# Optimization experiments

Hardware: AMD Instinct MI355X
Metric: run time of the kernel (lower is better)

The kernel has to match this reference:

```python
import jax, jax.numpy as jnp
import numpy as np

B, L, D = 2, 2048, 1024
H = 16          # num_heads == num_key_value_heads
FD = 16         # feature_dim (q/k head dim)
HD = D // H     # head_dim = 64 (v head dim)
EPS = 1e-5


def setup_inputs() -> dict:
    key = jax.random.key(0)
    k0, k1, k2, k3, k4 = jax.random.split(key, 5)
    scale = 0.02
    return {
        "hidden_states": jax.random.normal(k0, (B, L, D), jnp.float32),
        "Wq": jax.random.normal(k1, (D, H * FD), jnp.float32) * scale,
        "Wk": jax.random.normal(k2, (D, H * FD), jnp.float32) * scale,
        "Wv": jax.random.normal(k3, (D, H * HD), jnp.float32) * scale,
        "Wo": jax.random.normal(k4, (H * HD, D), jnp.float32) * scale,
    }


def reference(hidden_states, Wq, Wk, Wv, Wo):
    # projections (bias-free), split heads: b l (h d) -> b h l d
    q = (hidden_states @ Wq).reshape(B, L, H, FD).transpose(0, 2, 1, 3)
    k = (hidden_states @ Wk).reshape(B, L, H, FD).transpose(0, 2, 1, 3)
    v = (hidden_states @ Wv).reshape(B, L, H, HD).transpose(0, 2, 1, 3)

    # parallel_rebased: squared-dot-product kernel attention, causal,
    # row-normalized by the kernel sum (use_scale=True, use_normalize=True)
    qk_scale = FD ** -0.5
    s = jnp.einsum('bhqd,bhkd->bhqk', q * qk_scale, k)
    s = s * s  # quadratic feature map: (q.k)^2
    causal = jnp.tril(jnp.ones((L, L), dtype=bool))
    s = jnp.where(causal, s, 0.0)
    z = jnp.sum(s, axis=-1)  # [B,H,L]
    o = jnp.einsum('bhqk,bhkd->bhqd', s, v) / (z[..., None] + EPS)

    # merge heads: b h l d -> b l (h d), output projection
    o = o.transpose(0, 2, 1, 3).reshape(B, L, H * HD)
    return o @ Wo
```

## Files before the change

kernel.cpp:

```cpp
#include <hip/hip_runtime.h>
#include <hip/hip_bf16.h>

#define BB 2
#define LL 2048
#define DD 1024
#define HH 16
#define FD 16
#define HD 64
#define EPS 1e-5f
#define RQKV 1536
#define NFIX 4

typedef __attribute__((ext_vector_type(4))) float f32x4;
typedef __attribute__((ext_vector_type(8))) _Float16 f16x8;
typedef __attribute__((ext_vector_type(4))) _Float16 f16x4;

__global__ __launch_bounds__(256) void cast_hs(
    const float* __restrict__ src, _Float16* __restrict__ dst, int n) {
  int idx = (blockIdx.x * 256 + threadIdx.x) * 16;
  if (idx >= n) return;
#pragma unroll
  for (int half = 0; half < 2; half++) {
    float4 a = *(const float4*)(src + idx + half * 8);
    float4 b = *(const float4*)(src + idx + half * 8 + 4);
    f16x8 p = {(_Float16)a.x, (_Float16)a.y, (_Float16)a.z, (_Float16)a.w,
               (_Float16)b.x, (_Float16)b.y, (_Float16)b.z, (_Float16)b.w};
    *(f16x8*)(dst + idx + half * 8) = p;
  }
}

__global__ __launch_bounds__(256) void transpose_qkv(
    const float* __restrict__ Wq, const float* __restrict__ Wk,
    const float* __restrict__ Wv, _Float16* __restrict__ dst) {
  __shared__ _Float16 s[32][40];
  const int ct = blockIdx.x % 48, kt = blockIdx.x / 48;
  const float* src;
  int n0, ncol, drow;
  if (ct < 8) { src = Wq; n0 = ct * 32; ncol = 256; drow = n0; }
  else if (ct < 16) { src = Wk; n0 = (ct - 8) * 32; ncol = 256; drow = 256 + n0; }
  else { src = Wv; n0 = (ct - 16) * 32; ncol = 1024; drow = 512 + n0; }
  const int k0 = kt * 32;
  const int tid = threadIdx.x;
  {
    int r = tid >> 3, c = (tid & 7) * 4;
    float4 v = *(const float4*)(src + (size_t)(k0 + r) * ncol + n0 + c);
    f16x4 p = {(_Float16)v.x, (_Float16)v.y, (_Float16)v.z, (_Float16)v.w};
    *(f16x4*)&s[r][c] = p;
  }
  __syncthreads();
  {
    int n = tid >> 3, kk = (tid & 7) * 4;
    f16x4 o = {s[kk + 0][n], s[kk + 1][n], s[kk + 2][n], s[kk + 3][n]};
    *(f16x4*)(dst + (size_t)(drow + n) * DD + k0 + kk) = o;
  }
}

__global__ __launch_bounds__(256) void transpose_cast(
    const float* __restrict__ src, _Float16* __restrict__ dst, int K, int N) {
  __shared__ _Float16 s[32][40];
  const int n0 = blockIdx.x * 32, k0 = blockIdx.y * 32;
  const int tid = threadIdx.x;
  {
    int r = tid >> 3, c = (tid & 7) * 4;
    float4 v = *(const float4*)(src + (size_t)(k0 + r) * N + n0 + c);
    f16x4 p = {(_Float16)v.x, (_Float16)v.y, (_Float16)v.z, (_Float16)v.w};
    *(f16x4*)&s[r][c] = p;
  }
  __syncthreads();
  {
    int n = tid >> 3, kk = (tid & 7) * 4;
    f16x4 o = {s[kk + 0][n], s[kk + 1][n], s[kk + 2][n], s[kk + 3][n]};
    *(f16x4*)(dst + (size_t)(n0 + n) * K + k0 + kk) = o;
  }
}

template <typename OutT>
__global__ __launch_bounds__(256) void gemm_f16(
    const _Float16* __restrict__ A, const _Float16* __restrict__ Bt,
    OutT* __restrict__ C, int M, int N, int K) {
  constexpr int LDT = 72;
  __shared__ __attribute__((aligned(16))) _Float16 sA[128 * LDT];
  __shared__ __attribute__((aligned(16))) _Float16 sB[128 * LDT];
  const int tid = threadIdx.x;
  const int m0 = blockIdx.y * 128, n0 = blockIdx.x * 128;
  const int w = tid >> 6, lane = tid & 63, quad = lane >> 4, l16 = lane & 15;
  const int wm = (w >> 1) * 64, wn = (w & 1) * 64;

  const int sr = tid >> 1, sh = (tid & 1) * 32;
  const _Float16* Ag = A + (size_t)(m0 + sr) * K + sh;
  const _Float16* Bg = Bt + (size_t)(n0 + sr) * K + sh;
  _Float16* sAw = &sA[sr * LDT + sh];
  _Float16* sBw = &sB[sr * LDT + sh];

  f32x4 acc[4][4];
#pragma unroll
  for (int i = 0; i < 4; i++)
#pragma unroll
    for (int j = 0; j < 4; j++) acc[i][j] = (f32x4){0.f, 0.f, 0.f, 0.f};

  f16x8 ar[4], br[4];
  auto LOAD = [&](int k0) {
#pragma unroll
    for (int i = 0; i < 4; i++) {
      ar[i] = *(const f16x8*)(Ag + k0 + i * 8);
      br[i] = *(const f16x8*)(Bg + k0 + i * 8);
    }
  };
  LOAD(0);

  for (int k0 = 0; k0 < K; k0 += 64) {
    __syncthreads();
#pragma unroll
    for (int i = 0; i < 4; i++) {
      *(f16x8*)(sAw + i * 8) = ar[i];
      *(f16x8*)(sBw + i * 8) = br[i];
    }
    __syncthreads();
    if (k0 + 64 < K) LOAD(k0 + 64);

#pragma unroll
    for (int s = 0; s < 2; s++) {
      f16x8 af[4], bf[4];
#pragma unroll
      for (int i = 0; i < 4; i++)
        af[i] = *(const f16x8*)&sA[(wm + i * 16 + l16) * LDT + s * 32 + quad * 8];
#pragma unroll
      for (int j = 0; j < 4; j++)
        bf[j] = *(const f16x8*)&sB[(wn + j * 16 + l16) * LDT + s * 32 + quad * 8];
#pragma unroll
      for (int i = 0; i < 4; i++)
#pragma unroll
        for (int j = 0; j < 4; j++)
          acc[i][j] = __builtin_amdgcn_mfma_f32_16x16x32_f16(af[i], bf[j], acc[i][j], 0, 0, 0);
    }
  }

#pragma unroll
  for (int i = 0; i < 4; i++)
#pragma unroll
    for (int j = 0; j < 4; j++)
#pragma unroll
      for (int r = 0; r < 4; r++) {
        const int row = m0 + wm + i * 16 + quad * 4 + r;
        const int col = n0 + wn + j * 16 + l16;
        C[(size_t)row * N + col] = (OutT)acc[i][j][r];
      }
}

#define SK4 24
#define SV4 88
#define SS4 88

__global__ __launch_bounds__(256) void attn_mfma4(
    const _Float16* __restrict__ QKV, _Float16* __restrict__ O) {
  __shared__ __attribute__((aligned(16))) _Float16 sK[64 * SK4];
  __shared__ __attribute__((aligned(16))) _Float16 sVt[80 * SV4];
  __shared__ __attribute__((aligned(16))) _Float16 sS2[4 * 32 * SS4];

  const int bh = blockIdx.y;
  const int b = bh >> 4, h = bh & 15;
  const int qtA = blockIdx.x;
  const int qtB = 31 - qtA;
  const int tid = threadIdx.x;
  const int w = tid >> 6;
  const int lane = tid & 63;
  const int quad = lane >> 4;
  const int l16 = lane & 15;
  const int gqA = qtA * 64 + w * 16;
  const int gqB = qtB * 64 + w * 16;

  f16x8 qfragA = {}, qfragB = {};
  if (quad < 2) {
    qfragA = *(const f16x8*)(QKV +
        (size_t)(b * LL + gqA + l16) * RQKV + h * FD + quad * 8);
    qfragB = *(const f16x8*)(QKV +
        (size_t)(b * LL + gqB + l16) * RQKV + h * FD + quad * 8);
  }

  for (int t = tid; t < 16 * SV4; t += 256) {
    int r = t / SV4, c = t % SV4;
    sVt[64 * SV4 + t] = (_Float16)((r == 0 && c < 64) ? 1.0f : 0.0f);
  }
  __syncthreads();
  const f16x8 zf0 = *(const f16x8*)&sVt[(64 + l16) * SV4 + quad * 8];
  const f16x8 zf1 = *(const f16x8*)&sVt[(64 + l16) * SV4 + 32 + quad * 8];

  f32x4 oaccA[4], oaccB[4];
  f32x4 zaccA = (f32x4){0.f, 0.f, 0.f, 0.f};
  f32x4 zaccB = (f32x4){0.f, 0.f, 0.f, 0.f};
#pragma unroll
  for (int nt = 0; nt < 4; nt++) {
    oaccA[nt] = (f32x4){0.f, 0.f, 0.f, 0.f};
    oaccB[nt] = (f32x4){0.f, 0.f, 0.f, 0.f};
  }

  _Float16* sS2B = sS2 + w * 32 * SS4;
  _Float16* sS2A = sS2B + 16 * SS4;

  const int ktiles = qtB + 1;

  const int skey = tid >> 2, sfg = (tid & 3) * 4;
  uint2 kreg;
  f16x8 vreg0, vreg1;
  auto LOAD = [&](int kt) {
    kreg = *(const uint2*)(QKV +
        (size_t)(b * LL + kt * 64 + skey) * RQKV + 256 + h * FD + sfg);
    const _Float16* vp = QKV +
        (size_t)(b * LL + kt * 64 + lane) * RQKV + 512 + h * HD + w * 16;
    vreg0 = *(const f16x8*)vp;
    vreg1 = *(const f16x8*)(vp + 8);
  };
  LOAD(0);

  for (int kt = 0; kt < ktiles; kt++) {
    __syncthreads();
    *(uint2*)&sK[skey * SK4 + sfg] = kreg;
#pragma unroll
    for (int t = 0; t < 8; t++) sVt[(w * 16 + t) * SV4 + lane] = vreg0[t];
#pragma unroll
    for (int t = 0; t < 8; t++) sVt[(w * 16 + 8 + t) * SV4 + lane] = vreg1[t];
    __syncthreads();
    if (kt + 1 < ktiles) LOAD(kt + 1);

    const int k0 = kt * 64;
    const bool activeA = (kt <= qtA);

    f16x8 kf[4];
#pragma unroll
    for (int nt = 0; nt < 4; nt++) {
      f16x8 f = {};
      if (quad < 2) f = *(const f16x8*)&sK[(nt * 16 + l16) * SK4 + quad * 8];
      kf[nt] = f;
    }

    {
      const bool mask = (kt == qtB);
#pragma unroll
      for (int nt = 0; nt < 4; nt++) {
        f32x4 s = __builtin_amdgcn_mfma_f32_16x16x32_f16(
            qfragB, kf[nt], (f32x4){0.f, 0.f, 0.f, 0.f}, 0, 0, 0);
        const int gk = k0 + nt * 16 + l16;
#pragma unroll
        for (int r = 0; r < 4; r++) {
          float sv = s[r] * s[r] * 2.0f;
          if (mask) sv = (gk <= gqB + quad * 4 + r) ? sv : 0.0f;
          sS2B[(quad * 4 + r) * SS4 + nt * 16 + l16] = (_Float16)sv;
        }
      }
    }
    if (activeA) {
      const bool mask = (kt == qtA);
#pragma unroll
      for (int nt = 0; nt < 4; nt++) {
        f32x4 s = __builtin_amdgcn_mfma_f32_16x16x32_f16(
            qfragA, kf[nt], (f32x4){0.f, 0.f, 0.f, 0.f}, 0, 0, 0);
        const int gk = k0 + nt * 16 + l16;
#pragma unroll
        for (int r = 0; r < 4; r++) {
          float sv = s[r] * s[r] * 2.0f;
          if (mask) sv = (gk <= gqA + quad * 4 + r) ? sv : 0.0f;
          sS2A[(quad * 4 + r) * SS4 + nt * 16 + l16] = (_Float16)sv;
        }
      }
    }
    __asm__ volatile("s_waitcnt lgkmcnt(0)" ::: "memory");

    f16x8 afB0 = *(const f16x8*)&sS2B[l16 * SS4 + quad * 8];
    f16x8 afB1 = *(const f16x8*)&sS2B[l16 * SS4 + 32 + quad * 8];
    f16x8 afA0 = {}, afA1 = {};
    if (activeA) {
      afA0 = *(const f16x8*)&sS2A[l16 * SS4 + quad * 8];
      afA1 = *(const f16x8*)&sS2A[l16 * SS4 + 32 + quad * 8];
    }

#pragma unroll
    for (int nt = 0; nt < 4; nt++) {
      f16x8 vf0 = *(const f16x8*)&sVt[(nt * 16 + l16) * SV4 + quad * 8];
      f16x8 vf1 = *(const f16x8*)&sVt[(nt * 16 + l16) * SV4 + 32 + quad * 8];
      oaccB[nt] = __builtin_amdgcn_mfma_f32_16x16x32_f16(afB0, vf0, oaccB[nt], 0, 0, 0);
      oaccB[nt] = __builtin_amdgcn_mfma_f32_16x16x32_f16(afB1, vf1, oaccB[nt], 0, 0, 0);
      if (activeA) {
        oaccA[nt] = __builtin_amdgcn_mfma_f32_16x16x32_f16(afA0, vf0, oaccA[nt], 0, 0, 0);
        oaccA[nt] = __builtin_amdgcn_mfma_f32_16x16x32_f16(afA1, vf1, oaccA[nt], 0, 0, 0);
      }
    }
    zaccB = __builtin_amdgcn_mfma_f32_16x16x32_f16(afB0, zf0, zaccB, 0, 0, 0);
    zaccB = __builtin_amdgcn_mfma_f32_16x16x32_f16(afB1, zf1, zaccB, 0, 0, 0);
    if (activeA) {
      zaccA = __builtin_amdgcn_mfma_f32_16x16x32_f16(afA0, zf0, zaccA, 0, 0, 0);
      zaccA = __builtin_amdgcn_mfma_f32_16x16x32_f16(afA1, zf1, zaccA, 0, 0, 0);
    }
  }

  {
    float rz[4];
#pragma unroll
    for (int r = 0; r < 4; r++) {
      float zz = __shfl(zaccB[r], lane & 48);
      rz[r] = 1.0f / (zz + 32.0f * EPS);
    }
#pragma unroll
    for (int nt = 0; nt < 4; nt++)
#pragma unroll
      for (int r = 0; r < 4; r++) {
        const int gq = gqB + quad * 4 + r;
        O[(size_t)(b * LL + gq) * (HH * HD) + h * HD + nt * 16 + l16] =
            (_Float16)(oaccB[nt][r] * rz[r]);
      }
  }
  {
    float rz[4];
#pragma unroll
    for (int r = 0; r < 4; r++) {
      float zz = __shfl(zaccA[r], lane & 48);
      rz[r] = 1.0f / (zz + 32.0f * EPS);
    }
#pragma unroll
    for (int nt = 0; nt < 4; nt++)
#pragma unroll
      for (int r = 0; r < 4; r++) {
        const int gq = gqA + quad * 4 + r;
        O[(size_t)(b * LL + gq) * (HH * HD) + h * HD + nt * 16 + l16] =
            (_Float16)(oaccA[nt][r] * rz[r]);
      }
  }
}

__global__ __launch_bounds__(256) void early_qkv(
    const float* __restrict__ hs, const float* __restrict__ Wq,
    const float* __restrict__ Wk, const float* __restrict__ Wv,
    float* __restrict__ QKVe) {
  __shared__ float sHS[8][DD];
  __shared__ float part[8][8][32];
  const int tid = threadIdx.x;
  const int kg = tid >> 5, c = tid & 31;
  const int c0 = blockIdx.x * 32;

  for (int i = tid; i < 8 * (DD / 4); i += 256) {
    int e = i / (DD / 4), col4 = (i % (DD / 4)) * 4;
    int b = e >> 2, r = e & 3;
    *(float4*)&sHS[e][col4] =
        *(const float4*)(hs + (size_t)(b * LL + r) * DD + col4);
  }
  __syncthreads();

  const float* W;
  int col, ncol;
  if (c0 < 256) { W = Wq; col = c0 + c; ncol = 256; }
  else if (c0 < 512) { W = Wk; col = (c0 - 256) + c; ncol = 256; }
  else { W = Wv; col = (c0 - 512) + c; ncol = 1024; }

  float acc[8] = {};
  const int d0 = kg * 128;
#pragma unroll 4
  for (int d = d0; d < d0 + 128; d++) {
    float wv = W[(size_t)d * ncol + col];
#pragma unroll
    for (int e = 0; e < 8; e++) acc[e] += sHS[e][d] * wv;
  }
#pragma unroll
  for (int e = 0; e < 8; e++) part[kg][e][c] = acc[e];
  __syncthreads();

  {
    int e = tid >> 5;
    float t = 0.f;
#pragma unroll
    for (int g = 0; g < 8; g++) t += part[g][e][c];
    QKVe[(size_t)e * RQKV + c0 + c] = t;
  }
}

__global__ __launch_bounds__(256) void fix_final(
    const float* __restrict__ QKVe, _Float16* __restrict__ Oatt) {
  const int b = blockIdx.x >> 4, h = blockIdx.x & 15;
  const int tid = threadIdx.x;
  const int p = tid >> 6, d = tid & 63;

  float num = 0.f, z = 0.f;
  const float* qrow = QKVe + (size_t)(b * 4 + p) * RQKV + h * FD;
  for (int j = 0; j <= p; j++) {
    const float* krow = QKVe + (size_t)(b * 4 + j) * RQKV + 256 + h * FD;
    float s = 0.f;
#pragma unroll
    for (int f = 0; f < FD; f++) s += qrow[f] * krow[f];
    s *= 0.25f;
    s = s * s;
    z += s;
    num += s * QKVe[(size_t)(b * 4 + j) * RQKV + 512 + h * HD + d];
  }
  Oatt[(size_t)(b * LL + p) * (HH * HD) + h * HD + d] =
      (_Float16)(num / (z + EPS));
}

extern "C" void kernel_launch(void* const* d_in, const int* in_sizes, int n_in,
                              void* d_out, int out_size, void* d_ws, size_t ws_size,
                              hipStream_t stream) {
  const float* hs = (const float*)d_in[0];
  const float* Wq = (const float*)d_in[1];
  const float* Wk = (const float*)d_in[2];
  const float* Wv = (const float*)d_in[3];
  const float* Wo = (const float*)d_in[4];
  float* out = (float*)d_out;

  char* ws = (char*)d_ws;
  _Float16* WqkvT = (_Float16*)ws;
  _Float16* WoT   = (_Float16*)(ws + (3ull << 20));
  _Float16* HS16  = (_Float16*)(ws + (5ull << 20));
  _Float16* QKV   = (_Float16*)(ws + (13ull << 20));
  _Float16* Oatt  = (_Float16*)(ws + (25ull << 20));
  float*    QKVe  = (float*)(ws + (33ull << 20));

  const int M = BB * LL;

  cast_hs<<<dim3(M * DD / (256 * 16)), 256, 0, stream>>>(hs, HS16, M * DD);
  transpose_qkv<<<dim3(48 * 32), 256, 0, stream>>>(Wq, Wk, Wv, WqkvT);
  transpose_cast<<<dim3(DD / 32, DD / 32), 256, 0, stream>>>(Wo, WoT, DD, DD);

  early_qkv<<<dim3(RQKV / 32), 256, 0, stream>>>(hs, Wq, Wk, Wv, QKVe);

  gemm_f16<_Float16><<<dim3(RQKV / 128, M / 128), 256, 0, stream>>>(
      HS16, WqkvT, QKV, M, RQKV, DD);

  attn_mfma4<<<dim3(LL / 128, BB * HH), 256, 0, stream>>>(QKV, Oatt);

  fix_final<<<dim3(BB * HH), 256, 0, stream>>>(QKVe, Oatt);

  gemm_f16<float><<<dim3(DD / 128, M / 128), 256, 0, stream>>>(
      Oatt, WoT, out, M, DD, DD);
}
```

Measured before the change: 181.9 us.

## Load GEMM tiles directly into LDS via global_load_lds with swizzled layout

Both f16 GEMMs now copy A/B tiles straight from global memory into shared memory with the global_load_lds builtin, skipping the register staging step. The K step shrinks from 64 to 32 and the LDS layout becomes an unpadded blocked layout (8-row groups by 4 chunks), with precomputed fragment offsets. The old register prefetch of the next tile is gone, so each iteration waits on its own load behind a barrier and there is no longer any overlap of load and compute. The number of barriers per unit of K also doubles.

Result: slower. 206.4 us (+13.5%).

```diff
diff --git a/kernel.cpp b/kernel.cpp
--- a/kernel.cpp
+++ b/kernel.cpp
@@ -14,6 +14,12 @@
 typedef __attribute__((ext_vector_type(4))) float f32x4;
 typedef __attribute__((ext_vector_type(8))) _Float16 f16x8;
 typedef __attribute__((ext_vector_type(4))) _Float16 f16x4;
+
+static __device__ __forceinline__ void gld16(_Float16* lds, const _Float16* g) {
+  __builtin_amdgcn_global_load_lds(
+      (const __attribute__((address_space(1))) unsigned int*)g,
+      (__attribute__((address_space(3))) unsigned int*)lds, 16, 0, 0);
+}
 
 __global__ __launch_bounds__(256) void cast_hs(
     const float* __restrict__ src, _Float16* __restrict__ dst, int n) {
@@ -75,22 +81,35 @@
 }
 
 template <typename OutT>
-__global__ __launch_bounds__(256) void gemm_f16(
+__global__ __launch_bounds__(256) void gemm_lds(
     const _Float16* __restrict__ A, const _Float16* __restrict__ Bt,
     OutT* __restrict__ C, int M, int N, int K) {
-  constexpr int LDT = 72;
-  __shared__ __attribute__((aligned(16))) _Float16 sA[128 * LDT];
-  __shared__ __attribute__((aligned(16))) _Float16 sB[128 * LDT];
+  __shared__ __attribute__((aligned(16))) _Float16 sA[128 * 32];
+  __shared__ __attribute__((aligned(16))) _Float16 sB[128 * 32];
   const int tid = threadIdx.x;
   const int m0 = blockIdx.y * 128, n0 = blockIdx.x * 128;
   const int w = tid >> 6, lane = tid & 63, quad = lane >> 4, l16 = lane & 15;
   const int wm = (w >> 1) * 64, wn = (w & 1) * 64;
 
-  const int sr = tid >> 1, sh = (tid & 1) * 32;
-  const _Float16* Ag = A + (size_t)(m0 + sr) * K + sh;
-  const _Float16* Bg = Bt + (size_t)(n0 + sr) * K + sh;
-  _Float16* sAw = &sA[sr * LDT + sh];
-  _Float16* sBw = &sB[sr * LDT + sh];
+  const int row0 = ((tid) >> 5) * 8 + (tid & 7);
+  const int ch0 = (tid >> 3) & 3;
+  const _Float16* Ag0 = A + (size_t)(m0 + row0) * K + ch0 * 8;
+  const _Float16* Ag1 = Ag0 + (size_t)64 * K;
+  const _Float16* Bg0 = Bt + (size_t)(n0 + row0) * K + ch0 * 8;
+  const _Float16* Bg1 = Bg0 + (size_t)64 * K;
+  _Float16* lA0 = sA + w * 512;
+  _Float16* lA1 = sA + 2048 + w * 512;
+  _Float16* lB0 = sB + w * 512;
+  _Float16* lB1 = sB + 2048 + w * 512;
+
+  int aoff[4], boff[4];
+#pragma unroll
+  for (int i = 0; i < 4; i++) {
+    int row = wm + i * 16 + l16;
+    aoff[i] = (((row >> 3) << 5) + quad * 8 + (row & 7)) * 8;
+    row = wn + i * 16 + l16;
+    boff[i] = (((row >> 3) << 5) + quad * 8 + (row & 7)) * 8;
+  }
 
   f32x4 acc[4][4];
 #pragma unroll
@@ -98,41 +117,24 @@
 #pragma unroll
     for (int j = 0; j < 4; j++) acc[i][j] = (f32x4){0.f, 0.f, 0.f, 0.f};
 
-  f16x8 ar[4], br[4];
-  auto LOAD = [&](int k0) {
-#pragma unroll
-    for (int i = 0; i < 4; i++) {
-      ar[i] = *(const f16x8*)(Ag + k0 + i * 8);
-      br[i] = *(const f16x8*)(Bg + k0 + i * 8);
-    }
-  };
-  LOAD(0);
-
-  for (int k0 = 0; k0 < K; k0 += 64) {
+  for (int k0 = 0; k0 < K; k0 += 32) {
+    gld16(lA0, Ag0 + k0);
+    gld16(lA1, Ag1 + k0);
+    gld16(lB0, Bg0 + k0);
+    gld16(lB1, Bg1 + k0);
     __syncthreads();
-#pragma unroll
-    for (int i = 0; i < 4; i++) {
-      *(f16x8*)(sAw + i * 8) = ar[i];
-      *(f16x8*)(sBw + i * 8) = br[i];
-    }
+
+    f16x8 af[4], bf[4];
+#pragma unroll
+    for (int i = 0; i < 4; i++) af[i] = *(const f16x8*)&sA[aoff[i]];
+#pragma unroll
+    for (int j = 0; j < 4; j++) bf[j] = *(const f16x8*)&sB[boff[j]];
+#pragma unroll
+    for (int i = 0; i < 4; i++)
+#pragma unroll
+      for (int j = 0; j < 4; j++)
+        acc[i][j] = __builtin_amdgcn_mfma_f32_16x16x32_f16(af[i], bf[j], acc[i][j], 0, 0, 0);
     __syncthreads();
-    if (k0 + 64 < K) LOAD(k0 + 64);
-
-#pragma unroll
-    for (int s = 0; s < 2; s++) {
-      f16x8 af[4], bf[4];
-#pragma unroll
-      for (int i = 0; i < 4; i++)
-        af[i] = *(const f16x8*)&sA[(wm + i * 16 + l16) * LDT + s * 32 + quad * 8];
-#pragma unroll
-      for (int j = 0; j < 4; j++)
-        bf[j] = *(const f16x8*)&sB[(wn + j * 16 + l16) * LDT + s * 32 + quad * 8];
-#pragma unroll
-      for (int i = 0; i < 4; i++)
-#pragma unroll
-        for (int j = 0; j < 4; j++)
-          acc[i][j] = __builtin_amdgcn_mfma_f32_16x16x32_f16(af[i], bf[j], acc[i][j], 0, 0, 0);
-    }
   }
 
 #pragma unroll
@@ -419,13 +421,13 @@
 
   early_qkv<<<dim3(RQKV / 32), 256, 0, stream>>>(hs, Wq, Wk, Wv, QKVe);
 
-  gemm_f16<_Float16><<<dim3(RQKV / 128, M / 128), 256, 0, stream>>>(
+  gemm_lds<_Float16><<<dim3(RQKV / 128, M / 128), 256, 0, stream>>>(
       HS16, WqkvT, QKV, M, RQKV, DD);
 
   attn_mfma4<<<dim3(LL / 128, BB * HH), 256, 0, stream>>>(QKV, Oatt);
 
   fix_final<<<dim3(BB * HH), 256, 0, stream>>>(QKVe, Oatt);
 
-  gemm_f16<float><<<dim3(DD / 128, M / 128), 256, 0, stream>>>(
+  gemm_lds<float><<<dim3(DD / 128, M / 128), 256, 0, stream>>>(
       Oatt, WoT, out, M, DD, DD);
 }
```

## Shrink GEMM tile to 128x64 and use XOR-swizzled shared memory layout

Applied to the files above, without the earlier changes.

The f16 GEMM tile drops from 128x128 to 128x64 along N, and the launch grids are updated so each GEMM gets twice as many blocks. The padded LDS rows are replaced by an XOR swizzle to avoid bank conflicts without padding. Only half the threads load B. The aim is to fill more CUs on these small GEMMs (the QKV grid goes from 12x32 to 24x32 blocks) and cut LDS footprint, at the cost of less reuse of each A tile and more total global traffic for A.

After: 175.5 us. 3.5% less time.

```diff
diff --git a/kernel.cpp b/kernel.cpp
--- a/kernel.cpp
+++ b/kernel.cpp
@@ -78,67 +78,91 @@
 __global__ __launch_bounds__(256) void gemm_f16(
     const _Float16* __restrict__ A, const _Float16* __restrict__ Bt,
     OutT* __restrict__ C, int M, int N, int K) {
-  constexpr int LDT = 72;
-  __shared__ __attribute__((aligned(16))) _Float16 sA[128 * LDT];
-  __shared__ __attribute__((aligned(16))) _Float16 sB[128 * LDT];
-  const int tid = threadIdx.x;
-  const int m0 = blockIdx.y * 128, n0 = blockIdx.x * 128;
+  __shared__ __attribute__((aligned(16))) _Float16 sA[128 * 64];
+  __shared__ __attribute__((aligned(16))) _Float16 sB[64 * 64];
+  const int tid = threadIdx.x;
+  const int m0 = blockIdx.y * 128, n0 = blockIdx.x * 64;
   const int w = tid >> 6, lane = tid & 63, quad = lane >> 4, l16 = lane & 15;
-  const int wm = (w >> 1) * 64, wn = (w & 1) * 64;
-
-  const int sr = tid >> 1, sh = (tid & 1) * 32;
-  const _Float16* Ag = A + (size_t)(m0 + sr) * K + sh;
-  const _Float16* Bg = Bt + (size_t)(n0 + sr) * K + sh;
-  _Float16* sAw = &sA[sr * LDT + sh];
-  _Float16* sBw = &sB[sr * LDT + sh];
-
-  f32x4 acc[4][4];
+  const int wm = (w >> 1) * 64, wn = (w & 1) * 32;
+
+  const int sr = tid >> 1, p = tid & 1;
+  const int brow = (tid & 127) >> 1;
+  const _Float16* Ag = A + (size_t)(m0 + sr) * K + p * 32;
+  const _Float16* Bg = Bt + (size_t)(n0 + brow) * K + p * 32;
+  _Float16* sAw = &sA[sr * 64];
+  _Float16* sBw = &sB[brow * 64];
+  const int aswz = sr & 7, bswz = brow & 7;
+
+  f32x4 acc[4][2];
 #pragma unroll
   for (int i = 0; i < 4; i++)
 #pragma unroll
-    for (int j = 0; j < 4; j++) acc[i][j] = (f32x4){0.f, 0.f, 0.f, 0.f};
+    for (int j = 0; j < 2; j++) acc[i][j] = (f32x4){0.f, 0.f, 0.f, 0.f};
 
   f16x8 ar[4], br[4];
   auto LOAD = [&](int k0) {
 #pragma unroll
-    for (int i = 0; i < 4; i++) {
-      ar[i] = *(const f16x8*)(Ag + k0 + i * 8);
-      br[i] = *(const f16x8*)(Bg + k0 + i * 8);
+    for (int i = 0; i < 4; i++) ar[i] = *(const f16x8*)(Ag + k0 + i * 8);
+    if (tid < 128) {
+#pragma unroll
+      for (int i = 0; i < 4; i++) br[i] = *(const f16x8*)(Bg + k0 + i * 8);
     }
   };
   LOAD(0);
 
+  int aoff[4], boff[2];
+#pragma unroll
+  for (int i = 0; i < 4; i++) {
+    int row = wm + i * 16 + l16;
+    aoff[i] = row * 64 + ((quad ^ (row & 7)) * 8);
+  }
+#pragma unroll
+  for (int j = 0; j < 2; j++) {
+    int row = wn + j * 16 + l16;
+    boff[j] = row * 64 + ((quad ^ (row & 7)) * 8);
+  }
+
   for (int k0 = 0; k0 < K; k0 += 64) {
     __syncthreads();
 #pragma unroll
-    for (int i = 0; i < 4; i++) {
-      *(f16x8*)(sAw + i * 8) = ar[i];
-      *(f16x8*)(sBw + i * 8) = br[i];
+    for (int i = 0; i < 4; i++)
+      *(f16x8*)(sAw + (((4 * p + i) ^ aswz) * 8)) = ar[i];
+    if (tid < 128) {
+#pragma unroll
+      for (int i = 0; i < 4; i++)
+        *(f16x8*)(sBw + (((4 * p + i) ^ bswz) * 8)) = br[i];
     }
     __syncthreads();
     if (k0 + 64 < K) LOAD(k0 + 64);
 
 #pragma unroll
     for (int s = 0; s < 2; s++) {
-      f16x8 af[4], bf[4];
+      f16x8 af[4], bf[2];
+#pragma unroll
+      for (int i = 0; i < 4; i++) {
+        int row = wm + i * 16 + l16;
+        int col = ((s * 4 + quad) ^ (row & 7)) * 8;
+        af[i] = *(const f16x8*)&sA[row * 64 + col];
+      }
+#pragma unroll
+      for (int j = 0; j < 2; j++) {
+        int row = wn + j * 16 + l16;
+        int col = ((s * 4 + quad) ^ (row & 7)) * 8;
+        bf[j] = *(const f16x8*)&sB[row * 64 + col];
+      }
 #pragma unroll
       for (int i = 0; i < 4; i++)
-        af[i] = *(const f16x8*)&sA[(wm + i * 16 + l16) * LDT + s * 32 + quad * 8];
-#pragma unroll
-      for (int j = 0; j < 4; j++)
-        bf[j] = *(const f16x8*)&sB[(wn + j * 16 + l16) * LDT + s * 32 + quad * 8];
-#pragma unroll
-      for (int i = 0; i < 4; i++)
-#pragma unroll
-        for (int j = 0; j < 4; j++)
+#pragma unroll
+        for (int j = 0; j < 2; j++)
           acc[i][j] = __builtin_amdgcn_mfma_f32_16x16x32_f16(af[i], bf[j], acc[i][j], 0, 0, 0);
     }
   }
+  (void)aoff; (void)boff;
 
 #pragma unroll
   for (int i = 0; i < 4; i++)
 #pragma unroll
-    for (int j = 0; j < 4; j++)
+    for (int j = 0; j < 2; j++)
 #pragma unroll
       for (int r = 0; r < 4; r++) {
         const int row = m0 + wm + i * 16 + quad * 4 + r;
@@ -419,13 +443,13 @@
 
   early_qkv<<<dim3(RQKV / 32), 256, 0, stream>>>(hs, Wq, Wk, Wv, QKVe);
 
-  gemm_f16<_Float16><<<dim3(RQKV / 128, M / 128), 256, 0, stream>>>(
+  gemm_f16<_Float16><<<dim3(RQKV / 64, M / 128), 256, 0, stream>>>(
       HS16, WqkvT, QKV, M, RQKV, DD);
 
   attn_mfma4<<<dim3(LL / 128, BB * HH), 256, 0, stream>>>(QKV, Oatt);
 
   fix_final<<<dim3(BB * HH), 256, 0, stream>>>(QKVe, Oatt);
 
-  gemm_f16<float><<<dim3(DD / 128, M / 128), 256, 0, stream>>>(
+  gemm_f16<float><<<dim3(DD / 64, M / 128), 256, 0, stream>>>(
       Oatt, WoT, out, M, DD, DD);
 }
```
